# Performance work log

Measured on AMD Instinct MI355X. Metric: run time of the kernel, lower is better.

The kernel has to match this reference:

```python
import jax, jax.numpy as jnp
import numpy as np

B, H, L, D = 2, 16, 2048, 64


def setup_inputs() -> dict:
    key = jax.random.key(0)
    kq, kk, kv = jax.random.split(key, 3)
    q = jax.random.normal(kq, (B, H, L, D), dtype=jnp.float32)
    k = jax.random.normal(kk, (B, H, L, D), dtype=jnp.float32)
    v = jax.random.normal(kv, (B, H, L, D), dtype=jnp.float32)
    return {"q": q, "k": k, "v": v}


def reference(q, k, v):
    use_norm = True
    seq_len = q.shape[-2]
    scale = q.shape[-1] ** (-0.5)
    q = q * scale
    # [B, H, L, L] score matrix
    attn = jnp.einsum("bhqd,bhkd->bhqk", q, k)
    # 2nd-order Taylor expansion of exp: 1 + s + 0.5*s^2
    attn = 1.0 + attn + 0.5 * attn * attn
    # causal mask (lower-triangular kept)
    causal = jnp.tril(jnp.ones((seq_len, seq_len), dtype=bool))
    attn = jnp.where(causal, attn, 0.0)
    o = jnp.einsum("bhqk,bhkd->bhqd", attn, v)
    if use_norm:
        z = attn.sum(-1)
        o = o / (z[..., None] + 1e-06)
    return o
```

## Files before the change

kernel.cpp:

```cpp
#include <hip/hip_runtime.h>
#include <hip/hip_bf16.h>

typedef __bf16    bf16x8  __attribute__((ext_vector_type(8)));
typedef __bf16    bf16x4  __attribute__((ext_vector_type(4)));
typedef _Float16  half8   __attribute__((ext_vector_type(8)));
typedef _Float16  half4   __attribute__((ext_vector_type(4)));
typedef _Float16  half2   __attribute__((ext_vector_type(2)));
typedef float     floatx4 __attribute__((ext_vector_type(4)));

constexpr int Bc  = 2;
constexpr int Hc  = 16;
constexpr int Lc  = 2048;
constexpr int Dc  = 64;
constexpr int BHn = Bc * Hc;
constexpr int BM  = 128;
constexpr int BN  = 128;
constexpr int NQT = Lc / BM;
constexpr int LDK = 72;
constexpr int LDV = 136;
constexpr int KBYTES = BN * LDK * 2;
constexpr int VBYTES = Dc * LDV * 2;
constexpr int TILE_BYTES = KBYTES + VBYTES;
constexpr int TILE_GRANS = TILE_BYTES / 16;

static __device__ __forceinline__ half2 pack_f16(float a, float b) {
    return __builtin_bit_cast(half2, __builtin_amdgcn_cvt_pkrtz(a, b));
}

static __device__ __forceinline__ void dma16(const void* g, void* l) {
    __builtin_amdgcn_global_load_lds(
        (const __attribute__((address_space(1))) void*)g,
        (__attribute__((address_space(3))) void*)l, 16, 0, 0);
}

__global__ void prep(const float* __restrict__ kp, const float* __restrict__ vp,
                     char* __restrict__ kv) {
    const int bid = blockIdx.x, tid = threadIdx.x;
    if (bid < 1024) {
        const int R    = bid * 64 + (tid >> 2);
        const int s    = tid & 3;
        const int bh   = R >> 11;
        const int key  = R & 2047;
        const int tile = key >> 7;
        const int krow = key & 127;
        const float* src = kp + (size_t)R * 64 + s * 16;
        char* dst = kv + (size_t)(bh * 16 + tile) * TILE_BYTES + krow * 144 + s * 32;
        #pragma unroll
        for (int h = 0; h < 2; ++h) {
            floatx4 a = *(const floatx4*)(src + h * 8);
            floatx4 b = *(const floatx4*)(src + h * 8 + 4);
            bf16x8 o;
            o[0] = (__bf16)a[0]; o[1] = (__bf16)a[1]; o[2] = (__bf16)a[2]; o[3] = (__bf16)a[3];
            o[4] = (__bf16)b[0]; o[5] = (__bf16)b[1]; o[6] = (__bf16)b[2]; o[7] = (__bf16)b[3];
            *(bf16x8*)(dst + h * 16) = o;
        }
    } else {
        const int vb   = bid - 1024;
        const int bh   = vb >> 5, kt = vb & 31;
        const int key  = kt * 64 + (tid & 63);
        const int tile = kt >> 1;
        const int kwt  = (kt & 1) * 64 + (tid & 63);
        const int k5   = kwt & 31;
        const int pcol = (kwt & ~31) | (((k5 >> 2) & 3) * 8 + ((k5 >> 4) & 1) * 4 + (k5 & 3));
        const int d0   = (tid >> 6) * 16;
        const float* src = vp + ((size_t)bh * Lc + key) * Dc;
        _Float16* dst = (_Float16*)(kv + (size_t)(bh * 16 + tile) * TILE_BYTES + KBYTES);
        #pragma unroll
        for (int i = 0; i < 16; ++i) {
            const int d = d0 + i;
            dst[(size_t)d * LDV + pcol] = (_Float16)src[d];
        }
    }
}

__global__ __launch_bounds__(256, 2)
void taylor_attn(const float* __restrict__ qp, const char* __restrict__ kv,
                 float* __restrict__ op)
{
    __shared__ __align__(16) char smem[2 * TILE_BYTES];

    const int tid  = threadIdx.x;
    const int wv   = tid >> 6;
    const int lane = tid & 63;
    const int lm   = lane & 15;
    const int quad = lane >> 4;
    const int wq   = wv >> 1;
    const int wk   = wv & 1;

    const int cu    = (int)(blockIdx.x & 255);
    const int snd   = (int)(blockIdx.x >> 8);
    const int bh    = cu & 31;
    const int qslot = cu >> 5;
    const int qi    = snd ? qslot : (NQT - 1 - qslot);
    const int q0    = qi * BM;
    const int jmax  = qi;

    const float* qbase = qp + ((size_t)bh * Lc + q0) * Dc;
    const char*  kvbh  = kv + (size_t)bh * 16 * TILE_BYTES;

    floatx4 qv[8];
    const int r0 = tid >> 4, c4 = tid & 15;
    #pragma unroll
    for (int rep = 0; rep < 8; ++rep)
        qv[rep] = *(const floatx4*)(qbase + (r0 + rep * 16) * Dc + c4 * 4);

    {
        const char* src = kvbh;
        char* dst = smem;
        #pragma unroll
        for (int rep = 0; rep < 8; ++rep)
            dma16(src + (rep * 256 + tid) * 16, dst + (rep * 256 + tid) * 16);
        if (tid < 192)
            dma16(src + (2048 + tid) * 16, dst + (2048 + tid) * 16);
    }

    {
        __bf16* Qs = (__bf16*)(smem + TILE_BYTES);
        #pragma unroll
        for (int rep = 0; rep < 8; ++rep) {
            bf16x4 b;
            b[0] = (__bf16)qv[rep][0]; b[1] = (__bf16)qv[rep][1];
            b[2] = (__bf16)qv[rep][2]; b[3] = (__bf16)qv[rep][3];
            *(bf16x4*)&Qs[(r0 + rep * 16) * LDK + c4 * 4] = b;
        }
    }
    asm volatile("s_waitcnt lgkmcnt(0)" ::: "memory");
    __builtin_amdgcn_s_barrier();

    bf16x8 qa[4][2];
    {
        const __bf16* Qs = (const __bf16*)(smem + TILE_BYTES);
        #pragma unroll
        for (int st = 0; st < 4; ++st)
            #pragma unroll
            for (int kf = 0; kf < 2; ++kf)
                qa[st][kf] = *(const bf16x8*)&Qs[(64 * wq + 16 * st + lm) * LDK + kf * 32 + quad * 8];
    }
    asm volatile("s_waitcnt lgkmcnt(0)" ::: "memory");
    __builtin_amdgcn_s_barrier();

    floatx4 oacc[4][4] = {};
    floatx4 zacc[4]    = {};

    const half8 ones = {(_Float16)1.f, (_Float16)1.f, (_Float16)1.f, (_Float16)1.f,
                        (_Float16)1.f, (_Float16)1.f, (_Float16)1.f, (_Float16)1.f};
    const half2 c8  = {(_Float16)0.125f, (_Float16)0.125f};
    const half2 c1  = {(_Float16)1.f,    (_Float16)1.f};
    const half2 ch  = {(_Float16)0.5f,   (_Float16)0.5f};

    for (int j = 0; j <= jmax; ++j) {
        const int cur = j & 1;
        const __bf16*   Kc = (const __bf16*)(smem + cur * TILE_BYTES);
        const _Float16* Vc = (const _Float16*)(smem + cur * TILE_BYTES + KBYTES);

        if (j < jmax) {
            const char* src = kvbh + (size_t)(j + 1) * TILE_BYTES;
            char* dst = smem + (cur ^ 1) * TILE_BYTES;
            #pragma unroll
            for (int rep = 0; rep < 8; ++rep)
                dma16(src + (rep * 256 + tid) * 16, dst + (rep * 256 + tid) * 16);
            if (tid < 192)
                dma16(src + (2048 + tid) * 16, dst + (2048 + tid) * 16);
            if (wv < 3) asm volatile("s_waitcnt vmcnt(9)" ::: "memory");
            else        asm volatile("s_waitcnt vmcnt(8)" ::: "memory");
        } else {
            asm volatile("s_waitcnt vmcnt(0)" ::: "memory");
        }
        __builtin_amdgcn_s_barrier();

        const bool nm = (j == jmax);
        #pragma unroll
        for (int hf = 0; hf < 2; ++hf) {
            const int grp = 2 * wk + hf;

            floatx4 sacc[4][2] = {};
            #pragma unroll
            for (int kb4 = 0; kb4 < 2; ++kb4) {
                const int row0 = 16 * (4 * wk + 2 * hf + kb4);
                #pragma unroll
                for (int kf = 0; kf < 2; ++kf) {
                    bf16x8 ka = *(const bf16x8*)&Kc[(row0 + lm) * LDK + kf * 32 + quad * 8];
                    #pragma unroll
                    for (int st = 0; st < 4; ++st)
                        sacc[st][kb4] = __builtin_amdgcn_mfma_f32_16x16x32_bf16(ka, qa[st][kf], sacc[st][kb4], 0, 0, 0);
                }
            }

            half8 wf[4];
            #pragma unroll
            for (int st = 0; st < 4; ++st) {
                const int thr = q0 + 64 * wq + 16 * st + lm - j * BN;
                half2 wh[2][2];
                #pragma unroll
                for (int kb4 = 0; kb4 < 2; ++kb4) {
                    half2 s01 = pack_f16(sacc[st][kb4][0], sacc[st][kb4][1]);
                    half2 s23 = pack_f16(sacc[st][kb4][2], sacc[st][kb4][3]);
                    half2 a01 = s01 * c8 + c1;
                    half2 a23 = s23 * c8 + c1;
                    half2 w01 = a01 * (a01 * ch) + ch;
                    half2 w23 = a23 * (a23 * ch) + ch;
                    if (nm) {
                        const int i0 = 16 * (4 * wk + 2 * hf + kb4) + 4 * quad;
                        w01[0] = (i0 + 0 <= thr) ? w01[0] : (_Float16)0.f;
                        w01[1] = (i0 + 1 <= thr) ? w01[1] : (_Float16)0.f;
                        w23[0] = (i0 + 2 <= thr) ? w23[0] : (_Float16)0.f;
                        w23[1] = (i0 + 3 <= thr) ? w23[1] : (_Float16)0.f;
                    }
                    wh[kb4][0] = w01;
                    wh[kb4][1] = w23;
                }
                half4 lo = __builtin_shufflevector(wh[0][0], wh[0][1], 0, 1, 2, 3);
                half4 hi = __builtin_shufflevector(wh[1][0], wh[1][1], 0, 1, 2, 3);
                wf[st] = __builtin_shufflevector(lo, hi, 0, 1, 2, 3, 4, 5, 6, 7);
            }

            #pragma unroll
            for (int db = 0; db < 4; ++db) {
                half8 va = *(const half8*)&Vc[(16 * db + lm) * LDV + 32 * grp + 8 * quad];
                #pragma unroll
                for (int st = 0; st < 4; ++st)
                    oacc[st][db] = __builtin_amdgcn_mfma_f32_16x16x32_f16(va, wf[st], oacc[st][db], 0, 0, 0);
            }
            #pragma unroll
            for (int st = 0; st < 4; ++st)
                zacc[st] = __builtin_amdgcn_mfma_f32_16x16x32_f16(ones, wf[st], zacc[st], 0, 0, 0);
        }

        asm volatile("s_waitcnt lgkmcnt(0)" ::: "memory");
        __builtin_amdgcn_s_barrier();
    }

    float* Ored = (float*)smem;
    float* zred = (float*)(smem + 34816);
    if (wk) {
        #pragma unroll
        for (int st = 0; st < 4; ++st) {
            const int r = wq * 64 + 16 * st + lm;
            #pragma unroll
            for (int db = 0; db < 4; ++db)
                *(floatx4*)&Ored[(size_t)r * 68 + 16 * db + 4 * quad] = oacc[st][db];
            zred[r] = zacc[st][0];
        }
    }
    __syncthreads();
    if (!wk) {
        #pragma unroll
        for (int st = 0; st < 4; ++st) {
            const int r = wq * 64 + 16 * st + lm;
            const float inv = 1.0f / (zacc[st][0] + zred[r] + 1e-6f);
            const int qrow = q0 + 64 * wq + 16 * st + lm;
            float* orow = op + ((size_t)bh * Lc + qrow) * Dc;
            #pragma unroll
            for (int db = 0; db < 4; ++db) {
                floatx4 part = *(const floatx4*)&Ored[(size_t)r * 68 + 16 * db + 4 * quad];
                floatx4 t = (oacc[st][db] + part) * inv;
                *(floatx4*)&orow[16 * db + 4 * quad] = t;
            }
        }
    }
}

extern "C" void kernel_launch(void* const* d_in, const int* in_sizes, int n_in,
                              void* d_out, int out_size, void* d_ws, size_t ws_size,
                              hipStream_t stream) {
    const float* q = (const float*)d_in[0];
    const float* k = (const float*)d_in[1];
    const float* v = (const float*)d_in[2];
    float* o = (float*)d_out;

    char* kv = (char*)d_ws;

    prep<<<dim3(2048), dim3(256), 0, stream>>>(k, v, kv);
    taylor_attn<<<dim3(NQT * BHn), dim3(256), 0, stream>>>(q, kv, o);
}
```

Baseline: 117.6 us.

## Pair short and long query tiles per block to share K/V tile loads

Each 512-thread block now handles two query tiles of the same head, a short causal tile and its mirrored long tile. The two tiles share every K/V tile streamed into LDS, so global-to-LDS traffic is halved and the total causal work per block is balanced. Waves for the short tile sit idle but still take part in barriers once they pass their diagonal. Separately, the warp whose key half of the diagonal tile is entirely masked now skips that work. The cost is a larger block, idle waves for the short tile, and fewer, bigger blocks, which may hurt occupancy or latency hiding.

New measurement: 128.5 us. +9.3%, slower.

```diff
diff --git a/kernel.cpp b/kernel.cpp
--- a/kernel.cpp
+++ b/kernel.cpp
@@ -18,6 +18,7 @@
 constexpr int NQT = Lc / BM;
 constexpr int LDK = 72;
 constexpr int LDV = 136;
+constexpr int LDQ = 68;
 constexpr int KBYTES = BN * LDK * 2;
 constexpr int VBYTES = Dc * LDV * 2;
 constexpr int TILE_BYTES = KBYTES + VBYTES;
@@ -73,7 +74,7 @@
     }
 }
 
-__global__ __launch_bounds__(256, 2)
+__global__ __launch_bounds__(512, 2)
 void taylor_attn(const float* __restrict__ qp, const char* __restrict__ kv,
                  float* __restrict__ op)
 {
@@ -84,34 +85,39 @@
     const int lane = tid & 63;
     const int lm   = lane & 15;
     const int quad = lane >> 4;
-    const int wq   = wv >> 1;
+    const int grpB = wv >> 2;
+    const int wq   = (wv >> 1) & 1;
     const int wk   = wv & 1;
 
-    const int cu    = (int)(blockIdx.x & 255);
-    const int snd   = (int)(blockIdx.x >> 8);
-    const int bh    = cu & 31;
-    const int qslot = cu >> 5;
-    const int qi    = snd ? qslot : (NQT - 1 - qslot);
-    const int q0    = qi * BM;
-    const int jmax  = qi;
-
-    const float* qbase = qp + ((size_t)bh * Lc + q0) * Dc;
-    const char*  kvbh  = kv + (size_t)bh * 16 * TILE_BYTES;
+    const int bh    = (int)(blockIdx.x & 31);
+    const int qpair = (int)(blockIdx.x >> 5);
+    const int qiA   = qpair;
+    const int qiB   = NQT - 1 - qpair;
+    const int jmaxW = grpB ? qiB : qiA;
+    const int q0w   = jmaxW * BM;
+    const int jmaxB = qiB;
+
+    const char* kvbh = kv + (size_t)bh * 16 * TILE_BYTES;
 
     floatx4 qv[8];
     const int r0 = tid >> 4, c4 = tid & 15;
-    #pragma unroll
-    for (int rep = 0; rep < 8; ++rep)
-        qv[rep] = *(const floatx4*)(qbase + (r0 + rep * 16) * Dc + c4 * 4);
-
+    {
+        const float* qA = qp + ((size_t)bh * Lc + qiA * BM) * Dc;
+        const float* qB = qp + ((size_t)bh * Lc + qiB * BM) * Dc;
+        #pragma unroll
+        for (int rep = 0; rep < 4; ++rep)
+            qv[rep] = *(const floatx4*)(qA + (r0 + rep * 32) * Dc + c4 * 4);
+        #pragma unroll
+        for (int rep = 4; rep < 8; ++rep)
+            qv[rep] = *(const floatx4*)(qB + (r0 + (rep - 4) * 32) * Dc + c4 * 4);
+    }
     {
         const char* src = kvbh;
-        char* dst = smem;
-        #pragma unroll
-        for (int rep = 0; rep < 8; ++rep)
-            dma16(src + (rep * 256 + tid) * 16, dst + (rep * 256 + tid) * 16);
+        #pragma unroll
+        for (int rep = 0; rep < 4; ++rep)
+            dma16(src + (rep * 512 + tid) * 16, smem + (rep * 512 + tid) * 16);
         if (tid < 192)
-            dma16(src + (2048 + tid) * 16, dst + (2048 + tid) * 16);
+            dma16(src + (2048 + tid) * 16, smem + (2048 + tid) * 16);
     }
 
     {
@@ -121,7 +127,7 @@
             bf16x4 b;
             b[0] = (__bf16)qv[rep][0]; b[1] = (__bf16)qv[rep][1];
             b[2] = (__bf16)qv[rep][2]; b[3] = (__bf16)qv[rep][3];
-            *(bf16x4*)&Qs[(r0 + rep * 16) * LDK + c4 * 4] = b;
+            *(bf16x4*)&Qs[(r0 + rep * 32) * LDQ + c4 * 4] = b;
         }
     }
     asm volatile("s_waitcnt lgkmcnt(0)" ::: "memory");
@@ -134,7 +140,7 @@
         for (int st = 0; st < 4; ++st)
             #pragma unroll
             for (int kf = 0; kf < 2; ++kf)
-                qa[st][kf] = *(const bf16x8*)&Qs[(64 * wq + 16 * st + lm) * LDK + kf * 32 + quad * 8];
+                qa[st][kf] = *(const bf16x8*)&Qs[(128 * grpB + 64 * wq + 16 * st + lm) * LDQ + kf * 32 + quad * 8];
     }
     asm volatile("s_waitcnt lgkmcnt(0)" ::: "memory");
     __builtin_amdgcn_s_barrier();
@@ -148,90 +154,94 @@
     const half2 c1  = {(_Float16)1.f,    (_Float16)1.f};
     const half2 ch  = {(_Float16)0.5f,   (_Float16)0.5f};
 
-    for (int j = 0; j <= jmax; ++j) {
+    for (int j = 0; j <= jmaxB; ++j) {
         const int cur = j & 1;
         const __bf16*   Kc = (const __bf16*)(smem + cur * TILE_BYTES);
         const _Float16* Vc = (const _Float16*)(smem + cur * TILE_BYTES + KBYTES);
 
-        if (j < jmax) {
+        if (j < jmaxB) {
             const char* src = kvbh + (size_t)(j + 1) * TILE_BYTES;
             char* dst = smem + (cur ^ 1) * TILE_BYTES;
             #pragma unroll
-            for (int rep = 0; rep < 8; ++rep)
-                dma16(src + (rep * 256 + tid) * 16, dst + (rep * 256 + tid) * 16);
+            for (int rep = 0; rep < 4; ++rep)
+                dma16(src + (rep * 512 + tid) * 16, dst + (rep * 512 + tid) * 16);
             if (tid < 192)
                 dma16(src + (2048 + tid) * 16, dst + (2048 + tid) * 16);
-            if (wv < 3) asm volatile("s_waitcnt vmcnt(9)" ::: "memory");
-            else        asm volatile("s_waitcnt vmcnt(8)" ::: "memory");
+            if (wv < 3) asm volatile("s_waitcnt vmcnt(5)" ::: "memory");
+            else        asm volatile("s_waitcnt vmcnt(4)" ::: "memory");
         } else {
             asm volatile("s_waitcnt vmcnt(0)" ::: "memory");
         }
         __builtin_amdgcn_s_barrier();
 
-        const bool nm = (j == jmax);
-        #pragma unroll
-        for (int hf = 0; hf < 2; ++hf) {
-            const int grp = 2 * wk + hf;
-
-            floatx4 sacc[4][2] = {};
-            #pragma unroll
-            for (int kb4 = 0; kb4 < 2; ++kb4) {
-                const int row0 = 16 * (4 * wk + 2 * hf + kb4);
-                #pragma unroll
-                for (int kf = 0; kf < 2; ++kf) {
-                    bf16x8 ka = *(const bf16x8*)&Kc[(row0 + lm) * LDK + kf * 32 + quad * 8];
+        const bool nm = (j == jmaxW);
+        const bool active = (j <= jmaxW) && !(nm && wk && !wq);
+        if (active) {
+            #pragma unroll
+            for (int hf = 0; hf < 2; ++hf) {
+                const int grp = 2 * wk + hf;
+
+                floatx4 sacc[4][2] = {};
+                #pragma unroll
+                for (int kb4 = 0; kb4 < 2; ++kb4) {
+                    const int row0 = 16 * (4 * wk + 2 * hf + kb4);
+                    #pragma unroll
+                    for (int kf = 0; kf < 2; ++kf) {
+                        bf16x8 ka = *(const bf16x8*)&Kc[(row0 + lm) * LDK + kf * 32 + quad * 8];
+                        #pragma unroll
+                        for (int st = 0; st < 4; ++st)
+                            sacc[st][kb4] = __builtin_amdgcn_mfma_f32_16x16x32_bf16(ka, qa[st][kf], sacc[st][kb4], 0, 0, 0);
+                    }
+                }
+
+                half8 wf[4];
+                #pragma unroll
+                for (int st = 0; st < 4; ++st) {
+                    const int thr = q0w + 64 * wq + 16 * st + lm - j * BN;
+                    half2 wh[2][2];
+                    #pragma unroll
+                    for (int kb4 = 0; kb4 < 2; ++kb4) {
+                        half2 s01 = pack_f16(sacc[st][kb4][0], sacc[st][kb4][1]);
+                        half2 s23 = pack_f16(sacc[st][kb4][2], sacc[st][kb4][3]);
+                        half2 a01 = s01 * c8 + c1;
+                        half2 a23 = s23 * c8 + c1;
+                        half2 w01 = a01 * (a01 * ch) + ch;
+                        half2 w23 = a23 * (a23 * ch) + ch;
+                        if (nm) {
+                            const int i0 = 16 * (4 * wk + 2 * hf + kb4) + 4 * quad;
+                            w01[0] = (i0 + 0 <= thr) ? w01[0] : (_Float16)0.f;
+                            w01[1] = (i0 + 1 <= thr) ? w01[1] : (_Float16)0.f;
+                            w23[0] = (i0 + 2 <= thr) ? w23[0] : (_Float16)0.f;
+                            w23[1] = (i0 + 3 <= thr) ? w23[1] : (_Float16)0.f;
+                        }
+                        wh[kb4][0] = w01;
+                        wh[kb4][1] = w23;
+                    }
+                    half4 lo = __builtin_shufflevector(wh[0][0], wh[0][1], 0, 1, 2, 3);
+                    half4 hi = __builtin_shufflevector(wh[1][0], wh[1][1], 0, 1, 2, 3);
+                    wf[st] = __builtin_shufflevector(lo, hi, 0, 1, 2, 3, 4, 5, 6, 7);
+                }
+
+                #pragma unroll
+                for (int db = 0; db < 4; ++db) {
+                    half8 va = *(const half8*)&Vc[(16 * db + lm) * LDV + 32 * grp + 8 * quad];
                     #pragma unroll
                     for (int st = 0; st < 4; ++st)
-                        sacc[st][kb4] = __builtin_amdgcn_mfma_f32_16x16x32_bf16(ka, qa[st][kf], sacc[st][kb4], 0, 0, 0);
+                        oacc[st][db] = __builtin_amdgcn_mfma_f32_16x16x32_f16(va, wf[st], oacc[st][db], 0, 0, 0);
                 }
+                #pragma unroll
+                for (int st = 0; st < 4; ++st)
+                    zacc[st] = __builtin_amdgcn_mfma_f32_16x16x32_f16(ones, wf[st], zacc[st], 0, 0, 0);
             }
-
-            half8 wf[4];
-            #pragma unroll
-            for (int st = 0; st < 4; ++st) {
-                const int thr = q0 + 64 * wq + 16 * st + lm - j * BN;
-                half2 wh[2][2];
-                #pragma unroll
-                for (int kb4 = 0; kb4 < 2; ++kb4) {
-                    half2 s01 = pack_f16(sacc[st][kb4][0], sacc[st][kb4][1]);
-                    half2 s23 = pack_f16(sacc[st][kb4][2], sacc[st][kb4][3]);
-                    half2 a01 = s01 * c8 + c1;
-                    half2 a23 = s23 * c8 + c1;
-                    half2 w01 = a01 * (a01 * ch) + ch;
-                    half2 w23 = a23 * (a23 * ch) + ch;
-                    if (nm) {
-                        const int i0 = 16 * (4 * wk + 2 * hf + kb4) + 4 * quad;
-                        w01[0] = (i0 + 0 <= thr) ? w01[0] : (_Float16)0.f;
-                        w01[1] = (i0 + 1 <= thr) ? w01[1] : (_Float16)0.f;
-                        w23[0] = (i0 + 2 <= thr) ? w23[0] : (_Float16)0.f;
-                        w23[1] = (i0 + 3 <= thr) ? w23[1] : (_Float16)0.f;
-                    }
-                    wh[kb4][0] = w01;
-                    wh[kb4][1] = w23;
-                }
-                half4 lo = __builtin_shufflevector(wh[0][0], wh[0][1], 0, 1, 2, 3);
-                half4 hi = __builtin_shufflevector(wh[1][0], wh[1][1], 0, 1, 2, 3);
-                wf[st] = __builtin_shufflevector(lo, hi, 0, 1, 2, 3, 4, 5, 6, 7);
-            }
-
-            #pragma unroll
-            for (int db = 0; db < 4; ++db) {
-                half8 va = *(const half8*)&Vc[(16 * db + lm) * LDV + 32 * grp + 8 * quad];
-                #pragma unroll
-                for (int st = 0; st < 4; ++st)
-                    oacc[st][db] = __builtin_amdgcn_mfma_f32_16x16x32_f16(va, wf[st], oacc[st][db], 0, 0, 0);
-            }
-            #pragma unroll
-            for (int st = 0; st < 4; ++st)
-                zacc[st] = __builtin_amdgcn_mfma_f32_16x16x32_f16(ones, wf[st], zacc[st], 0, 0, 0);
         }
 
         asm volatile("s_waitcnt lgkmcnt(0)" ::: "memory");
         __builtin_amdgcn_s_barrier();
     }
 
-    float* Ored = (float*)smem;
-    float* zred = (float*)(smem + 34816);
+    float* base = (float*)(smem + grpB * TILE_BYTES);
+    float* Ored = base;
+    float* zred = (float*)((char*)base + 34816);
     if (wk) {
         #pragma unroll
         for (int st = 0; st < 4; ++st) {
@@ -248,7 +258,7 @@
         for (int st = 0; st < 4; ++st) {
             const int r = wq * 64 + 16 * st + lm;
             const float inv = 1.0f / (zacc[st][0] + zred[r] + 1e-6f);
-            const int qrow = q0 + 64 * wq + 16 * st + lm;
+            const int qrow = q0w + 64 * wq + 16 * st + lm;
             float* orow = op + ((size_t)bh * Lc + qrow) * Dc;
             #pragma unroll
             for (int db = 0; db < 4; ++db) {
@@ -271,5 +281,5 @@
     char* kv = (char*)d_ws;
 
     prep<<<dim3(2048), dim3(256), 0, stream>>>(k, v, kv);
-    taylor_attn<<<dim3(NQT * BHn), dim3(256), 0, stream>>>(q, kv, o);
-}
+    taylor_attn<<<dim3(BHn * NQT / 2), dim3(512), 0, stream>>>(q, kv, o);
+}
```

## Shrink attention tiles to 64x64 with one query strip per wave

Applied to the files above, without the earlier changes.

Query and key tiles drop from 128 to 64 rows. Each of the four waves now owns 16 query rows across the whole key tile, so the cross-wave LDS reduction of partial outputs and normalizers is gone. The launch grid doubles to 1024 blocks, scheduled in four rounds that alternate causal workload order, and launch bounds now request 4 blocks per CU. Smaller tiles cut LDS use and register pressure to raise occupancy and balance the causal triangle, at the cost of less K/V reuse per block and more barriers per key processed.

Measured after the change: 123.8 us. 5.3% more time.

```diff
diff --git a/kernel.cpp b/kernel.cpp
--- a/kernel.cpp
+++ b/kernel.cpp
@@ -13,14 +13,14 @@
 constexpr int Lc  = 2048;
 constexpr int Dc  = 64;
 constexpr int BHn = Bc * Hc;
-constexpr int BM  = 128;
-constexpr int BN  = 128;
+constexpr int BM  = 64;
+constexpr int BN  = 64;
 constexpr int NQT = Lc / BM;
 constexpr int LDK = 72;
-constexpr int LDV = 136;
-constexpr int KBYTES = BN * LDK * 2;
-constexpr int VBYTES = Dc * LDV * 2;
-constexpr int TILE_BYTES = KBYTES + VBYTES;
+constexpr int LDV = 72;
+constexpr int KB_T = BN * LDK * 2;
+constexpr int VB_T = Dc * LDV * 2;
+constexpr int TILE_BYTES = KB_T + VB_T;
 constexpr int TILE_GRANS = TILE_BYTES / 16;
 
 static __device__ __forceinline__ half2 pack_f16(float a, float b) {
@@ -41,10 +41,10 @@
         const int s    = tid & 3;
         const int bh   = R >> 11;
         const int key  = R & 2047;
-        const int tile = key >> 7;
-        const int krow = key & 127;
+        const int tile = key >> 6;
+        const int krow = key & 63;
         const float* src = kp + (size_t)R * 64 + s * 16;
-        char* dst = kv + (size_t)(bh * 16 + tile) * TILE_BYTES + krow * 144 + s * 32;
+        char* dst = kv + (size_t)(bh * 32 + tile) * TILE_BYTES + krow * 144 + s * 32;
         #pragma unroll
         for (int h = 0; h < 2; ++h) {
             floatx4 a = *(const floatx4*)(src + h * 8);
@@ -58,13 +58,12 @@
         const int vb   = bid - 1024;
         const int bh   = vb >> 5, kt = vb & 31;
         const int key  = kt * 64 + (tid & 63);
-        const int tile = kt >> 1;
-        const int kwt  = (kt & 1) * 64 + (tid & 63);
+        const int kwt  = tid & 63;
         const int k5   = kwt & 31;
-        const int pcol = (kwt & ~31) | (((k5 >> 2) & 3) * 8 + ((k5 >> 4) & 1) * 4 + (k5 & 3));
+        const int pcol = (kwt & 32) | (((k5 >> 2) & 3) * 8 + ((k5 >> 4) & 1) * 4 + (k5 & 3));
         const int d0   = (tid >> 6) * 16;
         const float* src = vp + ((size_t)bh * Lc + key) * Dc;
-        _Float16* dst = (_Float16*)(kv + (size_t)(bh * 16 + tile) * TILE_BYTES + KBYTES);
+        _Float16* dst = (_Float16*)(kv + (size_t)(bh * 32 + kt) * TILE_BYTES + KB_T);
         #pragma unroll
         for (int i = 0; i < 16; ++i) {
             const int d = d0 + i;
@@ -73,7 +72,7 @@
     }
 }
 
-__global__ __launch_bounds__(256, 2)
+__global__ __launch_bounds__(256, 4)
 void taylor_attn(const float* __restrict__ qp, const char* __restrict__ kv,
                  float* __restrict__ op)
 {
@@ -84,63 +83,59 @@
     const int lane = tid & 63;
     const int lm   = lane & 15;
     const int quad = lane >> 4;
-    const int wq   = wv >> 1;
-    const int wk   = wv & 1;
-
-    const int cu    = (int)(blockIdx.x & 255);
-    const int snd   = (int)(blockIdx.x >> 8);
-    const int bh    = cu & 31;
-    const int qslot = cu >> 5;
-    const int qi    = snd ? qslot : (NQT - 1 - qslot);
-    const int q0    = qi * BM;
-    const int jmax  = qi;
-
-    const float* qbase = qp + ((size_t)bh * Lc + q0) * Dc;
-    const char*  kvbh  = kv + (size_t)bh * 16 * TILE_BYTES;
-
-    floatx4 qv[8];
-    const int r0 = tid >> 4, c4 = tid & 15;
-    #pragma unroll
-    for (int rep = 0; rep < 8; ++rep)
-        qv[rep] = *(const floatx4*)(qbase + (r0 + rep * 16) * Dc + c4 * 4);
-
-    {
-        const char* src = kvbh;
-        char* dst = smem;
-        #pragma unroll
-        for (int rep = 0; rep < 8; ++rep)
-            dma16(src + (rep * 256 + tid) * 16, dst + (rep * 256 + tid) * 16);
-        if (tid < 192)
-            dma16(src + (2048 + tid) * 16, dst + (2048 + tid) * 16);
+
+    const int rnd = (int)(blockIdx.x >> 8);
+    const int s_  = (int)(blockIdx.x & 255);
+    const int bh  = s_ & 31;
+    const int t_  = s_ >> 5;
+    const int qi  = (rnd == 0) ? t_ : (rnd == 1) ? (15 - t_)
+                  : (rnd == 2) ? (16 + t_) : (31 - t_);
+    const int q0   = qi * BM;
+    const int jmax = qi;
+
+    const char* kvbh = kv + (size_t)bh * 32 * TILE_BYTES;
+
+    floatx4 qv[4];
+    const int r0 = tid >> 2, s4 = tid & 3;
+    {
+        const float* qbase = qp + ((size_t)bh * Lc + q0) * Dc;
+        #pragma unroll
+        for (int i = 0; i < 4; ++i)
+            qv[i] = *(const floatx4*)(qbase + r0 * 64 + s4 * 16 + i * 4);
+    }
+    {
+        #pragma unroll
+        for (int rep = 0; rep < 4; ++rep)
+            dma16(kvbh + (rep * 256 + tid) * 16, smem + (rep * 256 + tid) * 16);
+        if (tid < 128)
+            dma16(kvbh + (1024 + tid) * 16, smem + (1024 + tid) * 16);
     }
 
     {
         __bf16* Qs = (__bf16*)(smem + TILE_BYTES);
         #pragma unroll
-        for (int rep = 0; rep < 8; ++rep) {
+        for (int i = 0; i < 4; ++i) {
             bf16x4 b;
-            b[0] = (__bf16)qv[rep][0]; b[1] = (__bf16)qv[rep][1];
-            b[2] = (__bf16)qv[rep][2]; b[3] = (__bf16)qv[rep][3];
-            *(bf16x4*)&Qs[(r0 + rep * 16) * LDK + c4 * 4] = b;
+            b[0] = (__bf16)qv[i][0]; b[1] = (__bf16)qv[i][1];
+            b[2] = (__bf16)qv[i][2]; b[3] = (__bf16)qv[i][3];
+            *(bf16x4*)&Qs[r0 * LDK + s4 * 16 + i * 4] = b;
         }
     }
     asm volatile("s_waitcnt lgkmcnt(0)" ::: "memory");
     __builtin_amdgcn_s_barrier();
 
-    bf16x8 qa[4][2];
+    bf16x8 qa[2];
     {
         const __bf16* Qs = (const __bf16*)(smem + TILE_BYTES);
         #pragma unroll
-        for (int st = 0; st < 4; ++st)
-            #pragma unroll
-            for (int kf = 0; kf < 2; ++kf)
-                qa[st][kf] = *(const bf16x8*)&Qs[(64 * wq + 16 * st + lm) * LDK + kf * 32 + quad * 8];
+        for (int kf = 0; kf < 2; ++kf)
+            qa[kf] = *(const bf16x8*)&Qs[(16 * wv + lm) * LDK + kf * 32 + quad * 8];
     }
     asm volatile("s_waitcnt lgkmcnt(0)" ::: "memory");
     __builtin_amdgcn_s_barrier();
 
-    floatx4 oacc[4][4] = {};
-    floatx4 zacc[4]    = {};
+    floatx4 oacc[4] = {};
+    floatx4 zacc    = {};
 
     const half8 ones = {(_Float16)1.f, (_Float16)1.f, (_Float16)1.f, (_Float16)1.f,
                         (_Float16)1.f, (_Float16)1.f, (_Float16)1.f, (_Float16)1.f};
@@ -151,112 +146,87 @@
     for (int j = 0; j <= jmax; ++j) {
         const int cur = j & 1;
         const __bf16*   Kc = (const __bf16*)(smem + cur * TILE_BYTES);
-        const _Float16* Vc = (const _Float16*)(smem + cur * TILE_BYTES + KBYTES);
+        const _Float16* Vc = (const _Float16*)(smem + cur * TILE_BYTES + KB_T);
 
         if (j < jmax) {
             const char* src = kvbh + (size_t)(j + 1) * TILE_BYTES;
             char* dst = smem + (cur ^ 1) * TILE_BYTES;
             #pragma unroll
-            for (int rep = 0; rep < 8; ++rep)
+            for (int rep = 0; rep < 4; ++rep)
                 dma16(src + (rep * 256 + tid) * 16, dst + (rep * 256 + tid) * 16);
-            if (tid < 192)
-                dma16(src + (2048 + tid) * 16, dst + (2048 + tid) * 16);
-            if (wv < 3) asm volatile("s_waitcnt vmcnt(9)" ::: "memory");
-            else        asm volatile("s_waitcnt vmcnt(8)" ::: "memory");
+            if (tid < 128)
+                dma16(src + (1024 + tid) * 16, dst + (1024 + tid) * 16);
+            if (wv < 2) asm volatile("s_waitcnt vmcnt(5)" ::: "memory");
+            else        asm volatile("s_waitcnt vmcnt(4)" ::: "memory");
         } else {
             asm volatile("s_waitcnt vmcnt(0)" ::: "memory");
         }
         __builtin_amdgcn_s_barrier();
 
+        floatx4 sacc[4] = {};
+        #pragma unroll
+        for (int kb = 0; kb < 4; ++kb) {
+            #pragma unroll
+            for (int kf = 0; kf < 2; ++kf) {
+                bf16x8 ka = *(const bf16x8*)&Kc[(16 * kb + lm) * LDK + kf * 32 + quad * 8];
+                sacc[kb] = __builtin_amdgcn_mfma_f32_16x16x32_bf16(ka, qa[kf], sacc[kb], 0, 0, 0);
+            }
+        }
+
         const bool nm = (j == jmax);
-        #pragma unroll
-        for (int hf = 0; hf < 2; ++hf) {
-            const int grp = 2 * wk + hf;
-
-            floatx4 sacc[4][2] = {};
+        const int  thr = 16 * wv + lm;
+
+        half8 wf[2];
+        #pragma unroll
+        for (int g = 0; g < 2; ++g) {
+            half2 wh[2][2];
             #pragma unroll
             for (int kb4 = 0; kb4 < 2; ++kb4) {
-                const int row0 = 16 * (4 * wk + 2 * hf + kb4);
-                #pragma unroll
-                for (int kf = 0; kf < 2; ++kf) {
-                    bf16x8 ka = *(const bf16x8*)&Kc[(row0 + lm) * LDK + kf * 32 + quad * 8];
-                    #pragma unroll
-                    for (int st = 0; st < 4; ++st)
-                        sacc[st][kb4] = __builtin_amdgcn_mfma_f32_16x16x32_bf16(ka, qa[st][kf], sacc[st][kb4], 0, 0, 0);
+                const int kb = 2 * g + kb4;
+                half2 s01 = pack_f16(sacc[kb][0], sacc[kb][1]);
+                half2 s23 = pack_f16(sacc[kb][2], sacc[kb][3]);
+                half2 a01 = s01 * c8 + c1;
+                half2 a23 = s23 * c8 + c1;
+                half2 w01 = a01 * (a01 * ch) + ch;
+                half2 w23 = a23 * (a23 * ch) + ch;
+                if (nm) {
+                    const int i0 = 16 * kb + 4 * quad;
+                    w01[0] = (i0 + 0 <= thr) ? w01[0] : (_Float16)0.f;
+                    w01[1] = (i0 + 1 <= thr) ? w01[1] : (_Float16)0.f;
+                    w23[0] = (i0 + 2 <= thr) ? w23[0] : (_Float16)0.f;
+                    w23[1] = (i0 + 3 <= thr) ? w23[1] : (_Float16)0.f;
                 }
+                wh[kb4][0] = w01;
+                wh[kb4][1] = w23;
             }
-
-            half8 wf[4];
-            #pragma unroll
-            for (int st = 0; st < 4; ++st) {
-                const int thr = q0 + 64 * wq + 16 * st + lm - j * BN;
-                half2 wh[2][2];
-                #pragma unroll
-                for (int kb4 = 0; kb4 < 2; ++kb4) {
-                    half2 s01 = pack_f16(sacc[st][kb4][0], sacc[st][kb4][1]);
-                    half2 s23 = pack_f16(sacc[st][kb4][2], sacc[st][kb4][3]);
-                    half2 a01 = s01 * c8 + c1;
-                    half2 a23 = s23 * c8 + c1;
-                    half2 w01 = a01 * (a01 * ch) + ch;
-                    half2 w23 = a23 * (a23 * ch) + ch;
-                    if (nm) {
-                        const int i0 = 16 * (4 * wk + 2 * hf + kb4) + 4 * quad;
-                        w01[0] = (i0 + 0 <= thr) ? w01[0] : (_Float16)0.f;
-                        w01[1] = (i0 + 1 <= thr) ? w01[1] : (_Float16)0.f;
-                        w23[0] = (i0 + 2 <= thr) ? w23[0] : (_Float16)0.f;
-                        w23[1] = (i0 + 3 <= thr) ? w23[1] : (_Float16)0.f;
-                    }
-                    wh[kb4][0] = w01;
-                    wh[kb4][1] = w23;
-                }
-                half4 lo = __builtin_shufflevector(wh[0][0], wh[0][1], 0, 1, 2, 3);
-                half4 hi = __builtin_shufflevector(wh[1][0], wh[1][1], 0, 1, 2, 3);
-                wf[st] = __builtin_shufflevector(lo, hi, 0, 1, 2, 3, 4, 5, 6, 7);
+            half4 lo = __builtin_shufflevector(wh[0][0], wh[0][1], 0, 1, 2, 3);
+            half4 hi = __builtin_shufflevector(wh[1][0], wh[1][1], 0, 1, 2, 3);
+            wf[g] = __builtin_shufflevector(lo, hi, 0, 1, 2, 3, 4, 5, 6, 7);
+        }
+
+        #pragma unroll
+        for (int db = 0; db < 4; ++db) {
+            #pragma unroll
+            for (int g = 0; g < 2; ++g) {
+                half8 va = *(const half8*)&Vc[(16 * db + lm) * LDV + 32 * g + 8 * quad];
+                oacc[db] = __builtin_amdgcn_mfma_f32_16x16x32_f16(va, wf[g], oacc[db], 0, 0, 0);
             }
-
-            #pragma unroll
-            for (int db = 0; db < 4; ++db) {
-                half8 va = *(const half8*)&Vc[(16 * db + lm) * LDV + 32 * grp + 8 * quad];
-                #pragma unroll
-                for (int st = 0; st < 4; ++st)
-                    oacc[st][db] = __builtin_amdgcn_mfma_f32_16x16x32_f16(va, wf[st], oacc[st][db], 0, 0, 0);
-            }
-            #pragma unroll
-            for (int st = 0; st < 4; ++st)
-                zacc[st] = __builtin_amdgcn_mfma_f32_16x16x32_f16(ones, wf[st], zacc[st], 0, 0, 0);
-        }
+        }
+        #pragma unroll
+        for (int g = 0; g < 2; ++g)
+            zacc = __builtin_amdgcn_mfma_f32_16x16x32_f16(ones, wf[g], zacc, 0, 0, 0);
 
         asm volatile("s_waitcnt lgkmcnt(0)" ::: "memory");
         __builtin_amdgcn_s_barrier();
     }
 
-    float* Ored = (float*)smem;
-    float* zred = (float*)(smem + 34816);
-    if (wk) {
-        #pragma unroll
-        for (int st = 0; st < 4; ++st) {
-            const int r = wq * 64 + 16 * st + lm;
-            #pragma unroll
-            for (int db = 0; db < 4; ++db)
-                *(floatx4*)&Ored[(size_t)r * 68 + 16 * db + 4 * quad] = oacc[st][db];
-            zred[r] = zacc[st][0];
-        }
-    }
-    __syncthreads();
-    if (!wk) {
-        #pragma unroll
-        for (int st = 0; st < 4; ++st) {
-            const int r = wq * 64 + 16 * st + lm;
-            const float inv = 1.0f / (zacc[st][0] + zred[r] + 1e-6f);
-            const int qrow = q0 + 64 * wq + 16 * st + lm;
-            float* orow = op + ((size_t)bh * Lc + qrow) * Dc;
-            #pragma unroll
-            for (int db = 0; db < 4; ++db) {
-                floatx4 part = *(const floatx4*)&Ored[(size_t)r * 68 + 16 * db + 4 * quad];
-                floatx4 t = (oacc[st][db] + part) * inv;
-                *(floatx4*)&orow[16 * db + 4 * quad] = t;
-            }
-        }
+    const float inv = 1.0f / (zacc[0] + 1e-6f);
+    const int qrow = q0 + 16 * wv + lm;
+    float* orow = op + ((size_t)bh * Lc + qrow) * Dc;
+    #pragma unroll
+    for (int db = 0; db < 4; ++db) {
+        floatx4 t = oacc[db] * inv;
+        *(floatx4*)&orow[16 * db + 4 * quad] = t;
     }
 }
 
@@ -271,5 +241,5 @@
     char* kv = (char*)d_ws;
 
     prep<<<dim3(2048), dim3(256), 0, stream>>>(k, v, kv);
-    taylor_attn<<<dim3(NQT * BHn), dim3(256), 0, stream>>>(q, kv, o);
-}
+    taylor_attn<<<dim3(BHn * NQT), dim3(256), 0, stream>>>(q, kv, o);
+}
```
